# Kernel tuning notes

Hardware: AMD Instinct MI355X
Metric: run time of the kernel (lower is better)

## Reference

```python
import jax, jax.numpy as jnp
import numpy as np

LOCAL_W = 128
CHUNK_B = 8
N_LEVELS = 3
NEG = -1e30


def _sw_accum(q, k, v, W, gamma, scale):
    # Level 0: exact causal sliding window of W recent tokens with ALiBi decay.
    # Block-banded formulation: query block i only needs key blocks i-1 and i.
    B, H, N, d = q.shape
    nb = N // W
    qb = q.reshape(B, H, nb, W, d)
    kb = k.reshape(B, H, nb, W, d)
    vb = v.reshape(B, H, nb, W, d)
    k_prev = jnp.concatenate([jnp.zeros_like(kb[:, :, :1]), kb[:, :, :-1]], axis=2)
    v_prev = jnp.concatenate([jnp.zeros_like(vb[:, :, :1]), vb[:, :, :-1]], axis=2)
    kc = jnp.concatenate([k_prev, kb], axis=3)  # (B,H,nb,2W,d)
    vc = jnp.concatenate([v_prev, vb], axis=3)
    s = jnp.einsum('bhnpd,bhncd->bhnpc', qb, kc) * scale  # (B,H,nb,W,2W)
    p_idx = jnp.arange(W)[:, None]
    c_idx = jnp.arange(2 * W)[None, :]
    dist = (W + p_idx - c_idx).astype(s.dtype)  # i - j for key at col c
    band = (c_idx >= p_idx + 1) & (c_idx <= p_idx + W)  # j in [i-W+1, i]
    blk0 = (jnp.arange(nb)[:, None, None] > 0) | (c_idx >= W)[None]  # j >= 0
    mask = band[None] & blk0  # (nb, W, 2W)
    s = jnp.where(mask, s - gamma * dist, NEG)
    m = jnp.max(s, axis=-1)
    p = jnp.where(mask, jnp.exp(s - m[..., None]), 0.0)
    l = jnp.sum(p, axis=-1)
    o = jnp.einsum('bhnpc,bhncd->bhnpd', p, vc)
    return m.reshape(B, H, N), l.reshape(B, H, N), o.reshape(B, H, N, d)


def _hier(q, k_l, v_l, S, W, gamma, scale):
    # Level l: attend to mean-pooled chunks of effective size S = chunk_B**l.
    # A chunk is visible only when fully older than the sliding window.
    B, H, N, d = q.shape
    C = k_l.shape[2]
    s = jnp.einsum('bhnd,bhcd->bhnc', q, k_l) * scale  # (B,H,N,C)
    i = jnp.arange(N)[:, None]
    j_last = (jnp.arange(C)[None, :] + 1) * S - 1  # last raw token of chunk
    dist = (i - j_last).astype(s.dtype)
    visible = (i - j_last) >= W
    s = jnp.where(visible, s - gamma * dist, NEG)
    m = jnp.max(s, axis=-1)  # NEG when no chunk visible -> zero weight in merge
    p = jnp.where(visible, jnp.exp(s - m[..., None]), 0.0)
    return m, jnp.sum(p, axis=-1), jnp.einsum('bhnc,bhcd->bhnd', p, v_l)


def _forward(q, k, v, gammas):
    B, H, N, d = q.shape
    scale = 1.0 / float(np.sqrt(d))
    m, l, o = _sw_accum(q, k, v, LOCAL_W, gammas[0], scale)
    k_cur, v_cur = k, v
    for lvl in range(1, N_LEVELS + 1):
        n_chunks = k_cur.shape[2] // CHUNK_B
        if n_chunks == 0:
            continue
        usable = n_chunks * CHUNK_B
        k_cur = k_cur[:, :, :usable].reshape(B, H, n_chunks, CHUNK_B, d).mean(axis=3)
        v_cur = v_cur[:, :, :usable].reshape(B, H, n_chunks, CHUNK_B, d).mean(axis=3)
        m_l, l_l, o_l = _hier(q, k_cur, v_cur, CHUNK_B ** lvl, LOCAL_W, gammas[lvl], scale)
        mm = jnp.maximum(m, m_l)  # online-softmax merge across levels
        ea = jnp.exp(m - mm)
        eb = jnp.exp(m_l - mm)
        m = mm
        l = l * ea + l_l * eb
        o = o * ea[..., None] + o_l * eb[..., None]
    return o / jnp.clip(l, 1e-8)[..., None]


def setup_inputs() -> dict:
    key = jax.random.key(0)
    kq, kk, kv = jax.random.split(key, 3)
    B, H, N, d = 1, 16, 8192, 64
    q = jax.random.normal(kq, (B, H, N, d), dtype=jnp.float32)
    k = jax.random.normal(kk, (B, H, N, d), dtype=jnp.float32)
    v = jax.random.normal(kv, (B, H, N, d), dtype=jnp.float32)
    gammas = jnp.asarray([0.1 / CHUNK_B ** l for l in range(N_LEVELS + 1)], dtype=jnp.float32)
    return {"q": q, "k": k, "v": v, "gammas": gammas}


def reference(q, k, v, gammas):
    return _forward(q, k, v, gammas)
```

## Files before the change

### kernel.cpp

```cpp
#include <hip/hip_runtime.h>

#define NTOK 8192
#define NH 16
#define DD 64
#define NEGF -1e30f
#define LOG2E 1.4426950408889634f
#define CUT1 1024

typedef __attribute__((ext_vector_type(8))) short bf16x8;
typedef __attribute__((ext_vector_type(4))) float f32x4;

#define MFMA(a, b, c) __builtin_amdgcn_mfma_f32_16x16x32_bf16((a), (b), (c), 0, 0, 0)
#define EXP2(x) __builtin_amdgcn_exp2f(x)

static __device__ __forceinline__ unsigned short f2bf(float x) {
    union { float f; unsigned u; } c; c.f = x;
    unsigned r = (c.u + 0x7FFFu + ((c.u >> 16) & 1u)) >> 16;
    return (unsigned short)r;
}
static __device__ __forceinline__ float bf2f(unsigned short x) {
    union { unsigned u; float f; } c; c.u = ((unsigned)x) << 16;
    return c.f;
}

__global__ __launch_bounds__(256) void prep_kv1(const float* __restrict__ k, const float* __restrict__ v,
                                                unsigned short* __restrict__ Kb,
                                                unsigned short* __restrict__ vt,
                                                unsigned short* __restrict__ k1,
                                                unsigned short* __restrict__ vt1) {
    int h = blockIdx.x >> 7;
    int n0 = (blockIdx.x & 127) << 6;
    int tid = threadIdx.x;
    __shared__ unsigned short t[64][65];

    {
        int col = tid & 63;
        int rr = tid >> 6;
        const float* src = v + ((size_t)(h * NTOK + n0)) * DD;
#pragma unroll
        for (int r = 0; r < 16; ++r) {
            int row = rr + r * 4;
            t[col][row] = f2bf(src[(size_t)row * DD + col]);
        }
    }
    __syncthreads();
    {
        int d = tid >> 2, ch = tid & 3;
        union { unsigned short u[16]; uint4 q[2]; } tmp;
#pragma unroll
        for (int j = 0; j < 16; ++j) tmp.u[j] = t[d][ch * 16 + j];
        int b = (n0 >> 5) + (ch >> 1);
        unsigned short* dst = vt + ((size_t)(h * 256 + b)) * 2048 + d * 32 + (ch & 1) * 16;
        ((uint4*)dst)[0] = tmp.q[0];
        ((uint4*)dst)[1] = tmp.q[1];
    }
    {
        int dd = tid & 63;
        int cc = tid >> 6;
#pragma unroll
        for (int u = 0; u < 2; ++u) {
            int c8 = cc + u * 4;
            float s = 0.f;
#pragma unroll
            for (int r = 0; r < 8; ++r) s += bf2f(t[dd][8 * c8 + r]);
            int C = (n0 >> 3) + c8;
            vt1[((size_t)((h * 32 + (C >> 5)) * DD + dd)) * 32 + (C & 31)] = f2bf(s * 0.125f);
        }
    }
    __syncthreads();

    {
        int row = tid >> 2, cs = (tid & 3) * 16;
        const float* src = k + ((size_t)(h * NTOK + n0 + row)) * DD + cs;
        unsigned short* dst = Kb + ((size_t)(h * NTOK + n0 + row)) * DD + cs;
        float4 f0 = ((const float4*)src)[0], f1 = ((const float4*)src)[1];
        float4 f2 = ((const float4*)src)[2], f3 = ((const float4*)src)[3];
        union { unsigned short u[16]; uint4 q4[2]; } o;
        o.u[0] = f2bf(f0.x); o.u[1] = f2bf(f0.y); o.u[2] = f2bf(f0.z); o.u[3] = f2bf(f0.w);
        o.u[4] = f2bf(f1.x); o.u[5] = f2bf(f1.y); o.u[6] = f2bf(f1.z); o.u[7] = f2bf(f1.w);
        o.u[8] = f2bf(f2.x); o.u[9] = f2bf(f2.y); o.u[10] = f2bf(f2.z); o.u[11] = f2bf(f2.w);
        o.u[12] = f2bf(f3.x); o.u[13] = f2bf(f3.y); o.u[14] = f2bf(f3.z); o.u[15] = f2bf(f3.w);
        ((uint4*)dst)[0] = o.q4[0];
        ((uint4*)dst)[1] = o.q4[1];
#pragma unroll
        for (int j = 0; j < 16; ++j) t[cs + j][row] = o.u[j];
    }
    __syncthreads();
    {
        int dd = tid & 63;
        int cc = tid >> 6;
#pragma unroll
        for (int u = 0; u < 2; ++u) {
            int c8 = cc + u * 4;
            float s = 0.f;
#pragma unroll
            for (int r = 0; r < 8; ++r) s += bf2f(t[dd][8 * c8 + r]);
            int C = (n0 >> 3) + c8;
            k1[((size_t)(h * 1024 + C)) * DD + dd] = f2bf(s * 0.125f);
        }
    }
}

__global__ __launch_bounds__(256) void pool2_b(const unsigned short* __restrict__ k1,
                                               const unsigned short* __restrict__ vt1,
                                               unsigned short* __restrict__ k2,
                                               unsigned short* __restrict__ vt2) {
    int tid = blockIdx.x * blockDim.x + threadIdx.x;
    int d = tid & 63;
    int c = (tid >> 6) & 127;
    int h = tid >> 13;
    const unsigned short* kp = k1 + ((size_t)(h * 1024 + c * 8)) * DD + d;
    float ks = 0.f;
#pragma unroll
    for (int r = 0; r < 8; ++r) ks += bf2f(kp[(size_t)r * DD]);
    const unsigned short* vp = vt1 + ((size_t)((h * 32 + (c >> 2)) * DD + d)) * 32 + 8 * (c & 3);
    union { unsigned short u[8]; uint4 q; } vv;
    vv.q = *(const uint4*)(const void*)vp;
    float vs = 0.f;
#pragma unroll
    for (int j = 0; j < 8; ++j) vs += bf2f(vv.u[j]);
    k2[((size_t)(h * 128 + c)) * DD + d] = f2bf(ks * 0.125f);
    vt2[((size_t)((h * 4 + (c >> 5)) * DD + d)) * 32 + (c & 31)] = f2bf(vs * 0.125f);
}

__global__ __launch_bounds__(256) void pool3_b(const unsigned short* __restrict__ k2,
                                               const unsigned short* __restrict__ vt2,
                                               unsigned short* __restrict__ k3,
                                               unsigned short* __restrict__ vt3) {
    int tid = blockIdx.x * blockDim.x + threadIdx.x;
    int d = tid & 63;
    int c = (tid >> 6) & 31;
    int h = tid >> 11;
    float ks = 0.f, vs = 0.f;
    if (c < 16) {
        const unsigned short* kp = k2 + ((size_t)(h * 128 + c * 8)) * DD + d;
#pragma unroll
        for (int r = 0; r < 8; ++r) ks += bf2f(kp[(size_t)r * DD]);
        const unsigned short* vp = vt2 + ((size_t)((h * 4 + (c >> 2)) * DD + d)) * 32 + 8 * (c & 3);
        union { unsigned short u[8]; uint4 q; } vv;
        vv.q = *(const uint4*)(const void*)vp;
#pragma unroll
        for (int j = 0; j < 8; ++j) vs += bf2f(vv.u[j]);
        ks *= 0.125f; vs *= 0.125f;
    }
    k3[((size_t)(h * 32 + c)) * DD + d] = f2bf(ks);
    vt3[((size_t)(h * DD + d)) * 32 + c] = f2bf(vs);
}

struct KV32 { bf16x8 k0, k1, k2, k3, v0, v1, v2, v3; };

template<bool L0T, bool INIT>
__device__ __forceinline__ void grp64(
    int c0, int Qs, int lgS, float gp, float gps, float& m,
    const KV32& t, int g, int c,
    const bf16x8* q0, const bf16x8* q1,
    float* lac, f32x4 (*o)[4])
{
    f32x4 z = {0.f, 0.f, 0.f, 0.f};
    f32x4 sA[4], sB[4];
    __builtin_amdgcn_s_setprio(1);
#pragma unroll
    for (int tq = 0; tq < 4; ++tq) {
        sA[tq] = MFMA(t.k1, q1[tq], MFMA(t.k0, q0[tq], z));
        sB[tq] = MFMA(t.k3, q1[tq], MFMA(t.k2, q0[tq], z));
    }
    __builtin_amdgcn_s_setprio(0);

    float sv[4][8];
#pragma unroll
    for (int tq = 0; tq < 4; ++tq) {
        const int QsT = Qs + 16 * tq;
        const int i_q = QsT + c;
        const float negfb = gps * (float)(8 * g) + gp * (float)((1 << lgS) - 1) - gp * (float)i_q;
        bool fastT;
        if (L0T) {
            fastT = (c0 >= QsT - 112) && (c0 + 31 <= QsT);
        } else {
            int num = QsT - 128 - ((1 << lgS) - 1);
            fastT = (num >= 0) && (c0 + 31 <= (num >> lgS));
        }
        if (fastT) {
            float u0 = fmaf(gps, (float)c0, negfb);
            sv[tq][0] = sA[tq][0] + u0;
            sv[tq][1] = sA[tq][1] + fmaf(gps, 1.f, u0);
            sv[tq][2] = sA[tq][2] + fmaf(gps, 2.f, u0);
            sv[tq][3] = sA[tq][3] + fmaf(gps, 3.f, u0);
            sv[tq][4] = sB[tq][0] + fmaf(gps, 4.f, u0);
            sv[tq][5] = sB[tq][1] + fmaf(gps, 5.f, u0);
            sv[tq][6] = sB[tq][2] + fmaf(gps, 6.f, u0);
            sv[tq][7] = sB[tq][3] + fmaf(gps, 7.f, u0);
        } else {
#pragma unroll
            for (int r = 0; r < 4; ++r) {
                int cA = c0 + 8 * g + r, cB = cA + 4;
                int jA = L0T ? cA : (((cA + 1) << lgS) - 1);
                int jB = L0T ? cB : (((cB + 1) << lgS) - 1);
                int dA = i_q - jA, dB = i_q - jB;
                bool aA = L0T ? ((unsigned)dA <= 127u) : (dA >= 128);
                bool aB = L0T ? ((unsigned)dB <= 127u) : (dB >= 128);
                sv[tq][r]     = aA ? fmaf(-gp, (float)dA, sA[tq][r]) : NEGF;
                sv[tq][r + 4] = aB ? fmaf(-gp, (float)dB, sB[tq][r]) : NEGF;
            }
        }
    }

    if (INIT) {
        float tm = NEGF;
#pragma unroll
        for (int tq = 0; tq < 4; ++tq)
#pragma unroll
            for (int r = 0; r < 8; ++r) tm = fmaxf(tm, sv[tq][r]);
        tm = fmaxf(tm, __shfl_xor(tm, 1));
        tm = fmaxf(tm, __shfl_xor(tm, 2));
        tm = fmaxf(tm, __shfl_xor(tm, 4));
        tm = fmaxf(tm, __shfl_xor(tm, 8));
        tm = fmaxf(tm, __shfl_xor(tm, 16));
        tm = fmaxf(tm, __shfl_xor(tm, 32));
        m = tm;
    }

#pragma unroll
    for (int tq = 0; tq < 4; ++tq) {
        float p[8];
#pragma unroll
        for (int r = 0; r < 8; ++r) p[r] = EXP2(sv[tq][r] - m);
        lac[tq] += ((p[0] + p[1]) + (p[2] + p[3])) + ((p[4] + p[5]) + (p[6] + p[7]));
        union { unsigned u32[4]; bf16x8 v8; } pf;
#pragma unroll
        for (int j = 0; j < 4; ++j)
            asm("v_cvt_pk_bf16_f32 %0, %1, %2" : "=v"(pf.u32[j]) : "v"(p[2 * j]), "v"(p[2 * j + 1]));
        __builtin_amdgcn_s_setprio(1);
        o[tq][0] = MFMA(t.v0, pf.v8, o[tq][0]);
        o[tq][1] = MFMA(t.v1, pf.v8, o[tq][1]);
        o[tq][2] = MFMA(t.v2, pf.v8, o[tq][2]);
        o[tq][3] = MFMA(t.v3, pf.v8, o[tq][3]);
        __builtin_amdgcn_s_setprio(0);
    }
}

__global__ __launch_bounds__(64, 1) void attn_mfma(
    const float* __restrict__ q, const unsigned short* __restrict__ Kb,
    const unsigned short* __restrict__ Vtb,
    const unsigned short* __restrict__ K1, const unsigned short* __restrict__ Vt1,
    const unsigned short* __restrict__ K2, const unsigned short* __restrict__ Vt2,
    const unsigned short* __restrict__ K3, const unsigned short* __restrict__ Vt3,
    const float* __restrict__ gam, float* __restrict__ out) {
    const int lane = threadIdx.x;
    const int h = blockIdx.x & 15;
    const int qpos = 127 - (blockIdx.x >> 4);
    const int Qs = qpos << 6;
    const int g = lane >> 4;
    const int c = lane & 15;

    const float g0 = gam[0] * LOG2E, g1 = gam[1] * LOG2E;
    const float g2 = gam[2] * LOG2E, g3 = gam[3] * LOG2E;

    const size_t kperm = ((size_t)(8 * (c >> 2) + (c & 3))) * DD + g * 8;
    const unsigned short* KbH = Kb + (size_t)h * NTOK * DD + kperm;
    const unsigned short* VtH = Vtb + (size_t)h * 256 * 2048 + c * 32 + g * 8;
    const unsigned short* K1H = K1 + (size_t)h * 1024 * DD + kperm;
    const unsigned short* V1H = Vt1 + (size_t)h * 32 * 2048 + c * 32 + g * 8;
    const unsigned short* K2H = K2 + (size_t)h * 128 * DD + kperm;
    const unsigned short* V2H = Vt2 + (size_t)h * 4 * 2048 + c * 32 + g * 8;
    const unsigned short* K3H = K3 + (size_t)h * 32 * DD + kperm;
    const unsigned short* V3H = Vt3 + (size_t)h * 2048 + c * 32 + g * 8;

    auto LOADKV = [&](const unsigned short* Kh, const unsigned short* Vh, int c0) -> KV32 {
        KV32 r;
        const unsigned short* ka = Kh + (size_t)c0 * DD;
        r.k0 = *(const bf16x8*)(const void*)(ka);
        r.k1 = *(const bf16x8*)(const void*)(ka + 32);
        r.k2 = *(const bf16x8*)(const void*)(ka + 4 * DD);
        r.k3 = *(const bf16x8*)(const void*)(ka + 4 * DD + 32);
        const unsigned short* va = Vh + (size_t)(c0 >> 5) * 2048;
        r.v0 = *(const bf16x8*)(const void*)(va);
        r.v1 = *(const bf16x8*)(const void*)(va + 512);
        r.v2 = *(const bf16x8*)(const void*)(va + 1024);
        r.v3 = *(const bf16x8*)(const void*)(va + 1536);
        return r;
    };

    const float qsc = 0.125f * LOG2E;
    bf16x8 q0[4], q1[4];
#pragma unroll
    for (int tq = 0; tq < 4; ++tq) {
        const float* qr = q + ((size_t)(h * NTOK + Qs + 16 * tq + c)) * DD;
        float4 x0 = *(const float4*)(qr + g * 8),      x1 = *(const float4*)(qr + g * 8 + 4);
        float4 x2 = *(const float4*)(qr + 32 + g * 8), x3 = *(const float4*)(qr + 32 + g * 8 + 4);
        union { unsigned u32[4]; bf16x8 v8; } pA, pB;
        asm("v_cvt_pk_bf16_f32 %0, %1, %2" : "=v"(pA.u32[0]) : "v"(x0.x * qsc), "v"(x0.y * qsc));
        asm("v_cvt_pk_bf16_f32 %0, %1, %2" : "=v"(pA.u32[1]) : "v"(x0.z * qsc), "v"(x0.w * qsc));
        asm("v_cvt_pk_bf16_f32 %0, %1, %2" : "=v"(pA.u32[2]) : "v"(x1.x * qsc), "v"(x1.y * qsc));
        asm("v_cvt_pk_bf16_f32 %0, %1, %2" : "=v"(pA.u32[3]) : "v"(x1.z * qsc), "v"(x1.w * qsc));
        asm("v_cvt_pk_bf16_f32 %0, %1, %2" : "=v"(pB.u32[0]) : "v"(x2.x * qsc), "v"(x2.y * qsc));
        asm("v_cvt_pk_bf16_f32 %0, %1, %2" : "=v"(pB.u32[1]) : "v"(x2.z * qsc), "v"(x2.w * qsc));
        asm("v_cvt_pk_bf16_f32 %0, %1, %2" : "=v"(pB.u32[2]) : "v"(x3.x * qsc), "v"(x3.y * qsc));
        asm("v_cvt_pk_bf16_f32 %0, %1, %2" : "=v"(pB.u32[3]) : "v"(x3.z * qsc), "v"(x3.w * qsc));
        q0[tq] = pA.v8; q1[tq] = pB.v8;
    }

    f32x4 o[4][4];
#pragma unroll
    for (int tq = 0; tq < 4; ++tq)
#pragma unroll
        for (int db = 0; db < 4; ++db) o[tq][db] = (f32x4){0.f, 0.f, 0.f, 0.f};
    float lac[4] = {0.f, 0.f, 0.f, 0.f};
    float m = NEGF;

    {
        KV32 t = LOADKV(KbH, VtH, Qs + 32);
        grp64<true, true>(Qs + 32, Qs, 0, g0, g0, m, t, g, c, q0, q1, lac, o);
    }
    {
        int lo0 = Qs - 127; if (lo0 < 0) lo0 = 0; lo0 &= ~31;
        int c0 = Qs;
        while (c0 - 32 >= lo0) {
            KV32 a = LOADKV(KbH, VtH, c0);
            KV32 b = LOADKV(KbH, VtH, c0 - 32);
            grp64<true, false>(c0,      Qs, 0, g0, g0, m, a, g, c, q0, q1, lac, o);
            grp64<true, false>(c0 - 32, Qs, 0, g0, g0, m, b, g, c, q0, q1, lac, o);
            c0 -= 64;
        }
        if (c0 >= lo0) {
            KV32 a = LOADKV(KbH, VtH, c0);
            grp64<true, false>(c0, Qs, 0, g0, g0, m, a, g, c, q0, q1, lac, o);
        }
    }
    {
        int cm = Qs - 72;
        if (cm >= 0) {
            int top = (cm >> 3) & ~31;
            int lo = Qs - CUT1;
            lo = (lo <= 0) ? 0 : ((lo >> 3) & ~31);
            int c0 = top;
            while (c0 - 32 >= lo) {
                KV32 a = LOADKV(K1H, V1H, c0);
                KV32 b = LOADKV(K1H, V1H, c0 - 32);
                grp64<false, false>(c0,      Qs, 3, g1, g1 * 8.f, m, a, g, c, q0, q1, lac, o);
                grp64<false, false>(c0 - 32, Qs, 3, g1, g1 * 8.f, m, b, g, c, q0, q1, lac, o);
                c0 -= 64;
            }
            if (c0 >= lo) {
                KV32 a = LOADKV(K1H, V1H, c0);
                grp64<false, false>(c0, Qs, 3, g1, g1 * 8.f, m, a, g, c, q0, q1, lac, o);
            }
        }
    }
    {
        int cm2 = Qs - 128;
        if (cm2 >= 0) {
            int c0 = (cm2 >> 6) & ~31;
            while (c0 - 32 >= 0) {
                KV32 a = LOADKV(K2H, V2H, c0);
                KV32 b = LOADKV(K2H, V2H, c0 - 32);
                grp64<false, false>(c0,      Qs, 6, g2, g2 * 64.f, m, a, g, c, q0, q1, lac, o);
                grp64<false, false>(c0 - 32, Qs, 6, g2, g2 * 64.f, m, b, g, c, q0, q1, lac, o);
                c0 -= 64;
            }
            if (c0 >= 0) {
                KV32 a = LOADKV(K2H, V2H, c0);
                grp64<false, false>(c0, Qs, 6, g2, g2 * 64.f, m, a, g, c, q0, q1, lac, o);
            }
        }
    }
    {
        if (Qs >= 576) {
            KV32 t = LOADKV(K3H, V3H, 0);
            grp64<false, false>(0, Qs, 9, g3, g3 * 512.f, m, t, g, c, q0, q1, lac, o);
        }
    }

#pragma unroll
    for (int tq = 0; tq < 4; ++tq) {
        float lt = lac[tq] + __shfl_xor(lac[tq], 16);
        lt += __shfl_xor(lt, 32);
        float inv = 1.0f / fmaxf(lt, 1e-8f);
        float* orow = out + ((size_t)(h * NTOK + Qs + 16 * tq + c)) * DD;
#pragma unroll
        for (int db = 0; db < 4; ++db) {
            float4 x;
            x.x = o[tq][db][0] * inv; x.y = o[tq][db][1] * inv;
            x.z = o[tq][db][2] * inv; x.w = o[tq][db][3] * inv;
            *(float4*)(orow + db * 16 + 4 * g) = x;
        }
    }
}

extern "C" void kernel_launch(void* const* d_in, const int* in_sizes, int n_in,
                              void* d_out, int out_size, void* d_ws, size_t ws_size,
                              hipStream_t stream) {
    const float* q = (const float*)d_in[0];
    const float* k = (const float*)d_in[1];
    const float* v = (const float*)d_in[2];
    const float* gam = (const float*)d_in[3];
    float* out = (float*)d_out;

    char* w = (char*)d_ws;
    const size_t bigN = (size_t)NH * NTOK * DD * sizeof(unsigned short);
    unsigned short* Kbuf = (unsigned short*)w;  w += bigN;
    unsigned short* Vtb  = (unsigned short*)w;  w += bigN;
    unsigned short* K1   = (unsigned short*)w;  w += (size_t)NH * 1024 * DD * 2;
    unsigned short* Vt1  = (unsigned short*)w;  w += (size_t)NH * 1024 * DD * 2;
    unsigned short* K2   = (unsigned short*)w;  w += (size_t)NH * 128 * DD * 2;
    unsigned short* Vt2  = (unsigned short*)w;  w += (size_t)NH * 128 * DD * 2;
    unsigned short* K3   = (unsigned short*)w;  w += (size_t)NH * 32 * DD * 2;
    unsigned short* Vt3  = (unsigned short*)w;  w += (size_t)NH * 32 * DD * 2;

    prep_kv1<<<NH * (NTOK / 64), 256, 0, stream>>>(k, v, Kbuf, Vtb, K1, Vt1);
    pool2_b<<<NH * 128 * DD / 256, 256, 0, stream>>>(K1, Vt1, K2, Vt2);
    pool3_b<<<NH * 32 * DD / 256, 256, 0, stream>>>(K2, Vt2, K3, Vt3);

    attn_mfma<<<NH * 128, 64, 0, stream>>>(q, Kbuf, Vtb, K1, Vt1, K2, Vt2, K3, Vt3, gam, out);
}
```

Baseline: 72.32 us.

## Pre-permute level-0 K into MFMA fragment blocks and fuse pool2/pool3 kernels

The prep kernel now writes bf16 K in a per-32-token block layout matching the lane order of the MFMA fragments, so the attention kernel loads each K fragment with one contiguous 16-byte access per lane (lane*8 offset) instead of permuted row addresses. The two small pooling kernels for levels 2 and 3 are merged into one kernel per head that keeps level-2 results in shared memory to build level 3, removing a launch. The trade-off is that the fused pool kernel runs only 16 blocks, which gives it little parallelism.

```diff
diff --git a/kernel.cpp b/kernel.cpp
--- a/kernel.cpp
+++ b/kernel.cpp
@@ -72,7 +72,6 @@
     {
         int row = tid >> 2, cs = (tid & 3) * 16;
         const float* src = k + ((size_t)(h * NTOK + n0 + row)) * DD + cs;
-        unsigned short* dst = Kb + ((size_t)(h * NTOK + n0 + row)) * DD + cs;
         float4 f0 = ((const float4*)src)[0], f1 = ((const float4*)src)[1];
         float4 f2 = ((const float4*)src)[2], f3 = ((const float4*)src)[3];
         union { unsigned short u[16]; uint4 q4[2]; } o;
@@ -80,8 +79,14 @@
         o.u[4] = f2bf(f1.x); o.u[5] = f2bf(f1.y); o.u[6] = f2bf(f1.z); o.u[7] = f2bf(f1.w);
         o.u[8] = f2bf(f2.x); o.u[9] = f2bf(f2.y); o.u[10] = f2bf(f2.z); o.u[11] = f2bf(f2.w);
         o.u[12] = f2bf(f3.x); o.u[13] = f2bf(f3.y); o.u[14] = f2bf(f3.z); o.u[15] = f2bf(f3.w);
-        ((uint4*)dst)[0] = o.q4[0];
-        ((uint4*)dst)[1] = o.q4[1];
+        int grpb = (n0 >> 5) + (row >> 5);
+        int kk = row & 31;
+        int cw = ((kk >> 3) << 2) | (kk & 3);
+        int qd = ((kk >> 2) & 1) * 2 + (cs >= 32 ? 1 : 0);
+        int g0w = (cs & 31) >> 3;
+        unsigned short* blk = Kb + ((size_t)(h * 256 + grpb)) * 2048 + qd * 512;
+        *(uint4*)(blk + (g0w * 16 + cw) * 8) = o.q4[0];
+        *(uint4*)(blk + ((g0w + 1) * 16 + cw) * 8) = o.q4[1];
 #pragma unroll
         for (int j = 0; j < 16; ++j) t[cs + j][row] = o.u[j];
     }
@@ -101,50 +106,56 @@
     }
 }
 
-__global__ __launch_bounds__(256) void pool2_b(const unsigned short* __restrict__ k1,
-                                               const unsigned short* __restrict__ vt1,
-                                               unsigned short* __restrict__ k2,
-                                               unsigned short* __restrict__ vt2) {
-    int tid = blockIdx.x * blockDim.x + threadIdx.x;
-    int d = tid & 63;
-    int c = (tid >> 6) & 127;
-    int h = tid >> 13;
-    const unsigned short* kp = k1 + ((size_t)(h * 1024 + c * 8)) * DD + d;
-    float ks = 0.f;
-#pragma unroll
-    for (int r = 0; r < 8; ++r) ks += bf2f(kp[(size_t)r * DD]);
-    const unsigned short* vp = vt1 + ((size_t)((h * 32 + (c >> 2)) * DD + d)) * 32 + 8 * (c & 3);
-    union { unsigned short u[8]; uint4 q; } vv;
-    vv.q = *(const uint4*)(const void*)vp;
-    float vs = 0.f;
-#pragma unroll
-    for (int j = 0; j < 8; ++j) vs += bf2f(vv.u[j]);
-    k2[((size_t)(h * 128 + c)) * DD + d] = f2bf(ks * 0.125f);
-    vt2[((size_t)((h * 4 + (c >> 5)) * DD + d)) * 32 + (c & 31)] = f2bf(vs * 0.125f);
-}
-
-__global__ __launch_bounds__(256) void pool3_b(const unsigned short* __restrict__ k2,
-                                               const unsigned short* __restrict__ vt2,
-                                               unsigned short* __restrict__ k3,
-                                               unsigned short* __restrict__ vt3) {
-    int tid = blockIdx.x * blockDim.x + threadIdx.x;
-    int d = tid & 63;
-    int c = (tid >> 6) & 31;
-    int h = tid >> 11;
-    float ks = 0.f, vs = 0.f;
-    if (c < 16) {
-        const unsigned short* kp = k2 + ((size_t)(h * 128 + c * 8)) * DD + d;
+__global__ __launch_bounds__(256) void pool23(const unsigned short* __restrict__ k1,
+                                              const unsigned short* __restrict__ vt1,
+                                              unsigned short* __restrict__ k2,
+                                              unsigned short* __restrict__ vt2,
+                                              unsigned short* __restrict__ k3,
+                                              unsigned short* __restrict__ vt3) {
+    int h = blockIdx.x;
+    int tid = threadIdx.x;
+    __shared__ unsigned short sk2[128][64];
+    __shared__ unsigned short sv2[128][64];
+
+#pragma unroll
+    for (int i = 0; i < 32; ++i) {
+        int idx = tid + i * 256;
+        int d = idx & 63;
+        int c = idx >> 6;
+        const unsigned short* kp = k1 + ((size_t)(h * 1024 + c * 8)) * DD + d;
+        float ks = 0.f;
 #pragma unroll
         for (int r = 0; r < 8; ++r) ks += bf2f(kp[(size_t)r * DD]);
-        const unsigned short* vp = vt2 + ((size_t)((h * 4 + (c >> 2)) * DD + d)) * 32 + 8 * (c & 3);
+        const unsigned short* vp = vt1 + ((size_t)((h * 32 + (c >> 2)) * DD + d)) * 32 + 8 * (c & 3);
         union { unsigned short u[8]; uint4 q; } vv;
         vv.q = *(const uint4*)(const void*)vp;
+        float vs = 0.f;
 #pragma unroll
         for (int j = 0; j < 8; ++j) vs += bf2f(vv.u[j]);
-        ks *= 0.125f; vs *= 0.125f;
-    }
-    k3[((size_t)(h * 32 + c)) * DD + d] = f2bf(ks);
-    vt3[((size_t)(h * DD + d)) * 32 + c] = f2bf(vs);
+        unsigned short kb = f2bf(ks * 0.125f), vb = f2bf(vs * 0.125f);
+        k2[((size_t)(h * 128 + c)) * DD + d] = kb;
+        vt2[((size_t)((h * 4 + (c >> 5)) * DD + d)) * 32 + (c & 31)] = vb;
+        sk2[c][d] = kb;
+        sv2[c][d] = vb;
+    }
+    __syncthreads();
+#pragma unroll
+    for (int i = 0; i < 8; ++i) {
+        int idx = tid + i * 256;
+        int d = idx & 63;
+        int c = idx >> 6;
+        float ks = 0.f, vs = 0.f;
+        if (c < 16) {
+#pragma unroll
+            for (int j = 0; j < 8; ++j) {
+                ks += bf2f(sk2[c * 8 + j][d]);
+                vs += bf2f(sv2[c * 8 + j][d]);
+            }
+            ks *= 0.125f; vs *= 0.125f;
+        }
+        k3[((size_t)(h * 32 + c)) * DD + d] = f2bf(ks);
+        vt3[((size_t)(h * DD + d)) * 32 + c] = f2bf(vs);
+    }
 }
 
 struct KV32 { bf16x8 k0, k1, k2, k3, v0, v1, v2, v3; };
@@ -255,9 +266,9 @@
     const float g0 = gam[0] * LOG2E, g1 = gam[1] * LOG2E;
     const float g2 = gam[2] * LOG2E, g3 = gam[3] * LOG2E;
 
+    const unsigned short* KbB = Kb + (size_t)h * 256 * 2048 + lane * 8;
+    const unsigned short* VtH = Vtb + (size_t)h * 256 * 2048 + c * 32 + g * 8;
     const size_t kperm = ((size_t)(8 * (c >> 2) + (c & 3))) * DD + g * 8;
-    const unsigned short* KbH = Kb + (size_t)h * NTOK * DD + kperm;
-    const unsigned short* VtH = Vtb + (size_t)h * 256 * 2048 + c * 32 + g * 8;
     const unsigned short* K1H = K1 + (size_t)h * 1024 * DD + kperm;
     const unsigned short* V1H = Vt1 + (size_t)h * 32 * 2048 + c * 32 + g * 8;
     const unsigned short* K2H = K2 + (size_t)h * 128 * DD + kperm;
@@ -265,6 +276,20 @@
     const unsigned short* K3H = K3 + (size_t)h * 32 * DD + kperm;
     const unsigned short* V3H = Vt3 + (size_t)h * 2048 + c * 32 + g * 8;
 
+    auto LOADKV0 = [&](int c0) -> KV32 {
+        KV32 r;
+        const unsigned short* ka = KbB + (size_t)(c0 >> 5) * 2048;
+        r.k0 = *(const bf16x8*)(const void*)(ka);
+        r.k1 = *(const bf16x8*)(const void*)(ka + 512);
+        r.k2 = *(const bf16x8*)(const void*)(ka + 1024);
+        r.k3 = *(const bf16x8*)(const void*)(ka + 1536);
+        const unsigned short* va = VtH + (size_t)(c0 >> 5) * 2048;
+        r.v0 = *(const bf16x8*)(const void*)(va);
+        r.v1 = *(const bf16x8*)(const void*)(va + 512);
+        r.v2 = *(const bf16x8*)(const void*)(va + 1024);
+        r.v3 = *(const bf16x8*)(const void*)(va + 1536);
+        return r;
+    };
     auto LOADKV = [&](const unsigned short* Kh, const unsigned short* Vh, int c0) -> KV32 {
         KV32 r;
         const unsigned short* ka = Kh + (size_t)c0 * DD;
@@ -308,21 +333,21 @@
     float m = NEGF;
 
     {
-        KV32 t = LOADKV(KbH, VtH, Qs + 32);
+        KV32 t = LOADKV0(Qs + 32);
         grp64<true, true>(Qs + 32, Qs, 0, g0, g0, m, t, g, c, q0, q1, lac, o);
     }
     {
         int lo0 = Qs - 127; if (lo0 < 0) lo0 = 0; lo0 &= ~31;
         int c0 = Qs;
         while (c0 - 32 >= lo0) {
-            KV32 a = LOADKV(KbH, VtH, c0);
-            KV32 b = LOADKV(KbH, VtH, c0 - 32);
+            KV32 a = LOADKV0(c0);
+            KV32 b = LOADKV0(c0 - 32);
             grp64<true, false>(c0,      Qs, 0, g0, g0, m, a, g, c, q0, q1, lac, o);
             grp64<true, false>(c0 - 32, Qs, 0, g0, g0, m, b, g, c, q0, q1, lac, o);
             c0 -= 64;
         }
         if (c0 >= lo0) {
-            KV32 a = LOADKV(KbH, VtH, c0);
+            KV32 a = LOADKV0(c0);
             grp64<true, false>(c0, Qs, 0, g0, g0, m, a, g, c, q0, q1, lac, o);
         }
     }
@@ -407,8 +432,7 @@
     unsigned short* Vt3  = (unsigned short*)w;  w += (size_t)NH * 32 * DD * 2;
 
     prep_kv1<<<NH * (NTOK / 64), 256, 0, stream>>>(k, v, Kbuf, Vtb, K1, Vt1);
-    pool2_b<<<NH * 128 * DD / 256, 256, 0, stream>>>(K1, Vt1, K2, Vt2);
-    pool3_b<<<NH * 32 * DD / 256, 256, 0, stream>>>(K2, Vt2, K3, Vt3);
+    pool23<<<NH, 256, 0, stream>>>(K1, Vt1, K2, Vt2, K3, Vt3);
 
     attn_mfma<<<NH * 128, 64, 0, stream>>>(q, Kbuf, Vtb, K1, Vt1, K2, Vt2, K3, Vt3, gam, out);
 }
```

New measurement: 78.82 us. 1.09x slower.
